# Optimization experiments

Measured on AMD Instinct MI355X. Metric: run time of the kernel, lower is better.

Reference implementation:

```python
import jax, jax.numpy as jnp
import numpy as np

H = 2048       # hidden_size
I = 5504       # intermediate_size
E = 8          # num_experts
TOPK = 2       # num_experts_per_tok


def setup_inputs() -> dict:
    key = jax.random.key(0)
    ks = jax.random.split(key, 5)
    s = 0.02
    x = jax.random.normal(ks[0], (2, 2048, H), dtype=jnp.float32)
    router_w = jax.random.normal(ks[1], (E, H), dtype=jnp.float32) * s   # Linear weight [out,in]
    Wg = jax.random.normal(ks[2], (E, I, H), dtype=jnp.float32) * s      # gate_proj per expert
    Wu = jax.random.normal(ks[3], (E, I, H), dtype=jnp.float32) * s      # up_proj per expert
    Wd = jax.random.normal(ks[4], (E, H, I), dtype=jnp.float32) * s      # down_proj per expert
    return {"x": x, "router_w": router_w, "Wg": Wg, "Wu": Wu, "Wd": Wd}


def reference(x, router_w, Wg, Wu, Wd):
    B, S, Hh = x.shape
    xf = x.reshape(-1, Hh)                                  # [T, H]
    logits = xf @ router_w.T                                # [T, E]
    top_vals, top_idx = jax.lax.top_k(logits, TOPK)         # [T, K]
    top_w = jax.nn.softmax(top_vals, axis=-1)               # softmax over selected logits only
    # combine weight per (token, expert): zero if expert not selected
    combine = jnp.sum(jax.nn.one_hot(top_idx, E, dtype=xf.dtype) * top_w[..., None], axis=1)  # [T, E]

    out = jnp.zeros_like(xf)
    for e in range(E):  # fixed small expert loop (unrolled under jit)
        h = jax.nn.silu(xf @ Wg[e].T) * (xf @ Wu[e].T)      # [T, I]
        y = h @ Wd[e].T                                     # [T, H]
        out = out + combine[:, e:e + 1] * y
    return out.reshape(B, S, Hh)
```

## Files before the change

### kernel.cpp

```cpp
#include <hip/hip_runtime.h>
#include <cstdint>
#include <cstddef>

#define HDIM 2048
#define IDIM 5504
#define NEXP 8
#define NTOK 4096
#define NROWS (2 * NTOK)

#define NCT1 86
#define NRT1 10
#define NWG1 (NCT1 * NRT1 * NEXP)
#define NK1  (HDIM / 32)
#define NCT2 16
#define NRT2 10
#define NWG2 (NCT2 * NRT2 * NEXP)
#define NK2  (IDIM / 32)

typedef _Float16 half8 __attribute__((ext_vector_type(8)));
typedef _Float16 half4v __attribute__((ext_vector_type(4)));
typedef float floatx4 __attribute__((ext_vector_type(4)));

#define GLOAD16(g, l)                                                         \
  __builtin_amdgcn_global_load_lds(                                           \
      (const __attribute__((address_space(1))) void*)(g),                     \
      (__attribute__((address_space(3))) void*)(l), 16, 0, 0)

#define XH_OFF   0
#define HB_OFF   (XH_OFF + (size_t)NTOK * HDIM * 2)
#define BTOK_OFF (HB_OFF + (size_t)NROWS * IDIM * 2)
#define BW_OFF   (BTOK_OFF + 32768)
#define TOKP_OFF (BW_OFF + 32768)
#define TOKW_OFF (TOKP_OFF + 16384)
#define T2R_OFF  (TOKW_OFF + 32768)
#define META_OFF (T2R_OFF + 32768)
#define Y2_OFF   (META_OFF + 128)
#define WD16_OFF (Y2_OFF + (size_t)NROWS * HDIM * 2)


__global__ void cvt_w_kernel(const float4* __restrict__ w, half8* __restrict__ o, int n8) {
  int i = blockIdx.x * blockDim.x + threadIdx.x;
  int st = gridDim.x * blockDim.x;
  for (; i < n8; i += st) {
    float4 a = w[2 * i], b = w[2 * i + 1];
    o[i] = half8{ (_Float16)a.x, (_Float16)a.y, (_Float16)a.z, (_Float16)a.w,
                  (_Float16)b.x, (_Float16)b.y, (_Float16)b.z, (_Float16)b.w };
  }
}

__global__ void router_kernel(const float* __restrict__ x, const float* __restrict__ rw,
                              _Float16* __restrict__ xh,
                              int* __restrict__ tokp, float2* __restrict__ tokw,
                              int* __restrict__ cnt) {
  int t = blockIdx.x * 4 + (threadIdx.x >> 6);
  int lane = threadIdx.x & 63;
  const float4* xr = (const float4*)(x + (size_t)t * HDIM);
  _Float16* xhr = xh + (size_t)t * HDIM;
  float acc[NEXP];
#pragma unroll
  for (int e = 0; e < NEXP; ++e) acc[e] = 0.f;
#pragma unroll
  for (int it = 0; it < HDIM / 256; ++it) {
    float4 xv = xr[lane + 64 * it];
    half4v hv = { (_Float16)xv.x, (_Float16)xv.y, (_Float16)xv.z, (_Float16)xv.w };
    *(half4v*)(xhr + (lane + 64 * it) * 4) = hv;
#pragma unroll
    for (int e = 0; e < NEXP; ++e) {
      float4 wv = ((const float4*)(rw + (size_t)e * HDIM))[lane + 64 * it];
      acc[e] += xv.x * wv.x + xv.y * wv.y + xv.z * wv.z + xv.w * wv.w;
    }
  }
#pragma unroll
  for (int off = 32; off > 0; off >>= 1) {
#pragma unroll
    for (int e = 0; e < NEXP; ++e) acc[e] += __shfl_xor(acc[e], off);
  }
  if (lane == 0) {
    int e0 = 0; float v0 = acc[0];
#pragma unroll
    for (int e = 1; e < NEXP; ++e) {
      if (acc[e] > v0) { v0 = acc[e]; e0 = e; }
    }
    int e1 = -1; float v1 = -3.0e38f;
#pragma unroll
    for (int e = 0; e < NEXP; ++e) {
      if (e == e0) continue;
      if (acc[e] > v1) { v1 = acc[e]; e1 = e; }
    }
    float w0 = 1.f / (1.f + __expf(v1 - v0));
    tokp[t] = e0 | (e1 << 8);
    tokw[t] = make_float2(w0, 1.f - w0);
    atomicAdd(&cnt[e0], 1);
    atomicAdd(&cnt[e1], 1);
  }
}

__global__ void scan_kernel(const int* __restrict__ cnt, int* __restrict__ offp) {
  if (threadIdx.x == 0) {
    int s = 0;
    for (int e = 0; e < NEXP; ++e) { offp[e] = s; s += cnt[e]; }
    offp[NEXP] = s;
  }
}

__global__ void scatter_kernel(const int* __restrict__ tokp, const float2* __restrict__ tokw,
                               const int* __restrict__ offp, int* __restrict__ cursor,
                               int* __restrict__ btok, float* __restrict__ bw,
                               int* __restrict__ t2r) {
  int t = blockIdx.x * blockDim.x + threadIdx.x;
  if (t >= NTOK) return;
  int p = tokp[t];
  float2 w = tokw[t];
  int e0 = p & 0xff, e1 = (p >> 8) & 0xff;
  int r0 = offp[e0] + atomicAdd(&cursor[e0], 1);
  btok[r0] = t; bw[r0] = w.x; t2r[2 * t] = r0;
  int r1 = offp[e1] + atomicAdd(&cursor[e1], 1);
  btok[r1] = t; bw[r1] = w.y; t2r[2 * t + 1] = r1;
}

__global__ void combine_kernel(const _Float16* __restrict__ y2, const int* __restrict__ t2r,
                               const float2* __restrict__ tokw, float* __restrict__ out) {
  int idx = blockIdx.x * 256 + threadIdx.x;
  int t = idx >> 9, c = (idx & 511) * 4;
  int r0 = t2r[2 * t], r1 = t2r[2 * t + 1];
  float2 w = tokw[t];
  half4v v0 = *(const half4v*)(y2 + (size_t)r0 * HDIM + c);
  half4v v1 = *(const half4v*)(y2 + (size_t)r1 * HDIM + c);
  float4 o;
  o.x = w.x * (float)v0[0] + w.y * (float)v1[0];
  o.y = w.x * (float)v0[1] + w.y * (float)v1[1];
  o.z = w.x * (float)v0[2] + w.y * (float)v1[2];
  o.w = w.x * (float)v0[3] + w.y * (float)v1[3];
  *(float4*)(out + (size_t)t * HDIM + c) = o;
}

__global__ __launch_bounds__(256, 3) void stage1_kernel(
    const _Float16* __restrict__ xh, const float* __restrict__ Wg, const float* __restrict__ Wu,
    const int* __restrict__ offp, const int* __restrict__ btok, _Float16* __restrict__ hb) {
  int bid = blockIdx.x;
  int wg = (bid & 7) * (NWG1 / 8) + (bid >> 3);
  int rt = wg % NRT1;
  int ct = (wg / NRT1) % NCT1;
  int e  = wg / (NRT1 * NCT1);
  int base = offp[e];
  int ne = offp[e + 1] - base;
  if (rt * 128 >= ne) return;
  int valid = ne - rt * 128; if (valid > 128) valid = 128;
  int tid = threadIdx.x, lane = tid & 63, wave = tid >> 6;

  __shared__ __attribute__((aligned(16))) _Float16 As[2][128 * 32];
  __shared__ __attribute__((aligned(16))) _Float16 Bs[2][128 * 32];

  const char* abase = (const char*)xh;
  uint32_t aoffB[2];
  const float* bsrc[2];
  int bdstB[2];
  size_t eoff = (size_t)e * IDIM * HDIM;
#pragma unroll
  for (int i = 0; i < 2; ++i) {
    int L = wave * 128 + i * 64 + lane;
    int u = L >> 3, sc = (L & 7) ^ (u & 7);
    int r = 2 * u + (sc >> 2), q = sc & 3;
    int rr = (r < valid) ? r : (valid - 1);
    aoffB[i] = (uint32_t)(((uint32_t)btok[base + rt * 128 + rr] * HDIM + q * 8) * 2);
    const float* rp = (r < 64) ? (Wg + eoff + (size_t)(ct * 64 + r) * HDIM)
                               : (Wu + eoff + (size_t)(ct * 64 + (r - 64)) * HDIM);
    bsrc[i] = rp + q * 8;
    bdstB[i] = L * 16;
  }
  int adst0 = __builtin_amdgcn_readfirstlane(wave * 2048);

  int wm = wave >> 1, wn = wave & 1;
  int lrow = lane & 15, kg = lane >> 4;

  int aoff[4], boff[4];
#pragma unroll
  for (int mi = 0; mi < 4; ++mi) {
    int r = wm * 64 + mi * 16 + lrow;
    int u = r >> 1, cc = (r & 1) * 4 + kg;
    aoff[mi] = u * 64 + ((cc ^ (u & 7)) * 8);
  }
#pragma unroll
  for (int f = 0; f < 4; ++f) {
    int rb = (f < 2) ? (wn * 32 + f * 16 + lrow) : (64 + wn * 32 + (f - 2) * 16 + lrow);
    int u = rb >> 1, cc = (rb & 1) * 4 + kg;
    boff[f] = u * 64 + ((cc ^ (u & 7)) * 8);
  }

  floatx4 acc[4][4] = {};
  floatx4 bp[2][2];

  auto bload = [&](int t) {
#pragma unroll
    for (int i = 0; i < 2; ++i) {
      bp[i][0] = *(const floatx4*)(bsrc[i] + t * 32);
      bp[i][1] = *(const floatx4*)(bsrc[i] + t * 32 + 4);
    }
  };
  auto astage = [&](int t, int buf) {
    uint32_t kb = (uint32_t)t * 64u;
#pragma unroll
    for (int i = 0; i < 2; ++i)
      GLOAD16(abase + (aoffB[i] + kb), (char*)As[buf] + adst0 + i * 1024);
  };
  auto bwrite = [&](int buf) {
#pragma unroll
    for (int i = 0; i < 2; ++i) {
      half8 h = { (_Float16)bp[i][0].x, (_Float16)bp[i][0].y, (_Float16)bp[i][0].z, (_Float16)bp[i][0].w,
                  (_Float16)bp[i][1].x, (_Float16)bp[i][1].y, (_Float16)bp[i][1].z, (_Float16)bp[i][1].w };
      *(half8*)((char*)Bs[buf] + bdstB[i]) = h;
    }
  };
  auto compute = [&](int buf) {
    half8 af[4], bf[4];
#pragma unroll
    for (int mi = 0; mi < 4; ++mi) af[mi] = *(const half8*)&As[buf][aoff[mi]];
#pragma unroll
    for (int f = 0; f < 4; ++f) bf[f] = *(const half8*)&Bs[buf][boff[f]];
#pragma unroll
    for (int mi = 0; mi < 4; ++mi)
#pragma unroll
      for (int f = 0; f < 4; ++f)
        acc[mi][f] = __builtin_amdgcn_mfma_f32_16x16x32_f16(af[mi], bf[f], acc[mi][f], 0, 0, 0);
  };

  int cur = 0;
  bload(0);
  astage(0, 0);
  bwrite(0);
  __syncthreads();
#pragma unroll 2
  for (int t = 0; t < NK1 - 1; ++t) {
    bload(t + 1);
    astage(t + 1, cur ^ 1);
    compute(cur);
    bwrite(cur ^ 1);
    __syncthreads();
    cur ^= 1;
  }
  compute(cur);

  size_t hrow_base = (size_t)(base + rt * 128);
#pragma unroll
  for (int mi = 0; mi < 4; ++mi) {
#pragma unroll
    for (int j = 0; j < 4; ++j) {
      int r = wm * 64 + mi * 16 + kg * 4 + j;
      if (r < valid) {
#pragma unroll
        for (int f = 0; f < 2; ++f) {
          float g = acc[mi][f][j], u = acc[mi][f + 2][j];
          float hv = g / (1.f + __expf(-g)) * u;
          int c = ct * 64 + wn * 32 + f * 16 + lrow;
          hb[(hrow_base + r) * IDIM + c] = (_Float16)hv;
        }
      }
    }
  }
}

__global__ __launch_bounds__(256, 3) void stage2_kernel(
    const _Float16* __restrict__ hb, const _Float16* __restrict__ Wd16,
    const int* __restrict__ offp, _Float16* __restrict__ y2) {
  int bid = blockIdx.x;
  int wg = (bid & 7) * (NWG2 / 8) + (bid >> 3);
  int rt = wg % NRT2;
  int ct = (wg / NRT2) % NCT2;
  int e  = wg / (NRT2 * NCT2);
  int base = offp[e];
  int ne = offp[e + 1] - base;
  if (rt * 128 >= ne) return;
  int valid = ne - rt * 128; if (valid > 128) valid = 128;
  int tid = threadIdx.x, lane = tid & 63, wave = tid >> 6;

  __shared__ __attribute__((aligned(16))) _Float16 As[2][128 * 32];
  __shared__ __attribute__((aligned(16))) _Float16 Bs[2][128 * 32];

  const char* abase = (const char*)hb;
  const char* bbase = (const char*)(Wd16 + (size_t)e * HDIM * IDIM);

  uint32_t aoffB[2], boffB[2];
#pragma unroll
  for (int i = 0; i < 2; ++i) {
    int L = wave * 128 + i * 64 + lane;
    int u = L >> 3, sc = (L & 7) ^ (u & 7);
    int r = 2 * u + (sc >> 2), q = sc & 3;
    int rr = (r < valid) ? r : (valid - 1);
    aoffB[i] = (uint32_t)(((size_t)(base + rt * 128 + rr) * IDIM + (size_t)q * 8) * 2);
    boffB[i] = (uint32_t)(((size_t)(ct * 128 + r) * IDIM + (size_t)q * 8) * 2);
  }
  int adst0 = __builtin_amdgcn_readfirstlane(wave * 2048);

  int wm = wave >> 1, wn = wave & 1;
  int lrow = lane & 15, kg = lane >> 4;

  int aoff[4], boff[4];
#pragma unroll
  for (int mi = 0; mi < 4; ++mi) {
    int r = wm * 64 + mi * 16 + lrow;
    int u = r >> 1, cc = (r & 1) * 4 + kg;
    aoff[mi] = u * 64 + ((cc ^ (u & 7)) * 8);
  }
#pragma unroll
  for (int f = 0; f < 4; ++f) {
    int rb = wn * 64 + f * 16 + lrow;
    int u = rb >> 1, cc = (rb & 1) * 4 + kg;
    boff[f] = u * 64 + ((cc ^ (u & 7)) * 8);
  }

  floatx4 acc[4][4] = {};

  auto stage = [&](int t, int buf) {
    uint32_t kb = (uint32_t)t * 64u;
#pragma unroll
    for (int i = 0; i < 2; ++i) {
      GLOAD16(abase + (aoffB[i] + kb), (char*)As[buf] + adst0 + i * 1024);
      GLOAD16(bbase + (boffB[i] + kb), (char*)Bs[buf] + adst0 + i * 1024);
    }
  };
  auto compute = [&](int buf) {
    half8 af[4], bf[4];
#pragma unroll
    for (int mi = 0; mi < 4; ++mi) af[mi] = *(const half8*)&As[buf][aoff[mi]];
#pragma unroll
    for (int f = 0; f < 4; ++f) bf[f] = *(const half8*)&Bs[buf][boff[f]];
#pragma unroll
    for (int mi = 0; mi < 4; ++mi)
#pragma unroll
      for (int f = 0; f < 4; ++f)
        acc[mi][f] = __builtin_amdgcn_mfma_f32_16x16x32_f16(af[mi], bf[f], acc[mi][f], 0, 0, 0);
  };

  int cur = 0;
  stage(0, 0);
  __syncthreads();
#pragma unroll 2
  for (int t = 0; t < NK2 - 1; ++t) {
    stage(t + 1, cur ^ 1);
    compute(cur);
    __syncthreads();
    cur ^= 1;
  }
  compute(cur);

#pragma unroll
  for (int mi = 0; mi < 4; ++mi) {
#pragma unroll
    for (int j = 0; j < 4; ++j) {
      int r = wm * 64 + mi * 16 + kg * 4 + j;
      if (r < valid) {
        int grow = base + rt * 128 + r;
#pragma unroll
        for (int f = 0; f < 4; ++f) {
          int c = ct * 128 + wn * 64 + f * 16 + lrow;
          y2[(size_t)grow * HDIM + c] = (_Float16)acc[mi][f][j];
        }
      }
    }
  }
}

extern "C" void kernel_launch(void* const* d_in, const int* in_sizes, int n_in,
                              void* d_out, int out_size, void* d_ws, size_t ws_size,
                              hipStream_t stream) {
  const float* x  = (const float*)d_in[0];
  const float* rw = (const float*)d_in[1];
  const float* Wg = (const float*)d_in[2];
  const float* Wu = (const float*)d_in[3];
  const float* Wd = (const float*)d_in[4];
  float* out = (float*)d_out;

  char* ws = (char*)d_ws;
  _Float16* xh  = (_Float16*)(ws + XH_OFF);
  _Float16* hb  = (_Float16*)(ws + HB_OFF);
  int*      btok = (int*)(ws + BTOK_OFF);
  float*    bwv  = (float*)(ws + BW_OFF);
  int*      tokp = (int*)(ws + TOKP_OFF);
  float2*   tokw = (float2*)(ws + TOKW_OFF);
  int*      t2r  = (int*)(ws + T2R_OFF);
  int*      meta = (int*)(ws + META_OFF);
  _Float16* y2   = (_Float16*)(ws + Y2_OFF);
  _Float16* wd16 = (_Float16*)(ws + WD16_OFF);
  int* cnt = meta;
  int* offp = meta + 8;
  int* cursor = meta + 20;

  hipMemsetAsync(meta, 0, 128, stream);

  router_kernel<<<NTOK / 4, 256, 0, stream>>>(x, rw, xh, tokp, tokw, cnt);
  scan_kernel<<<1, 64, 0, stream>>>(cnt, offp);
  scatter_kernel<<<NTOK / 256, 256, 0, stream>>>(tokp, tokw, offp, cursor, btok, bwv, t2r);
  cvt_w_kernel<<<2048, 256, 0, stream>>>((const float4*)Wd, (half8*)wd16,
                                         NEXP * HDIM * IDIM / 8);

  stage1_kernel<<<NWG1, 256, 0, stream>>>(xh, Wg, Wu, offp, btok, hb);
  stage2_kernel<<<NWG2, 256, 0, stream>>>(hb, wd16, offp, y2);
  combine_kernel<<<NTOK * HDIM / 4 / 256, 256, 0, stream>>>(y2, t2r, tokw, out);
}
```

Measured before the change: 1.156 ms.

## Fuse Wd fp16 conversion into stage1 and widen stage2 tiles to 256 columns

Removes the separate Wd conversion kernel. Its grid-stride fp32-to-fp16 conversion now runs at the tail of every stage1 workgroup, including workgroups with no rows, so it overlaps with the GEMM work of other blocks. Stage2 moves to 512-thread blocks with 128x256 tiles, halving the column tiles, so each hidden-activation tile is reused across more output columns. The costs are more LDS per stage2 block, an aggressive launch bound of 6 blocks per CU, and extra memory traffic in stage1 competing with its GEMM loads.

```diff
diff --git a/kernel.cpp b/kernel.cpp
--- a/kernel.cpp
+++ b/kernel.cpp
@@ -12,10 +12,11 @@
 #define NRT1 10
 #define NWG1 (NCT1 * NRT1 * NEXP)
 #define NK1  (HDIM / 32)
-#define NCT2 16
+#define NCT2 8
 #define NRT2 10
 #define NWG2 (NCT2 * NRT2 * NEXP)
 #define NK2  (IDIM / 32)
+#define WDCH (NEXP * HDIM * IDIM / 8)
 
 typedef _Float16 half8 __attribute__((ext_vector_type(8)));
 typedef _Float16 half4v __attribute__((ext_vector_type(4)));
@@ -37,16 +38,6 @@
 #define Y2_OFF   (META_OFF + 128)
 #define WD16_OFF (Y2_OFF + (size_t)NROWS * HDIM * 2)
 
-
-__global__ void cvt_w_kernel(const float4* __restrict__ w, half8* __restrict__ o, int n8) {
-  int i = blockIdx.x * blockDim.x + threadIdx.x;
-  int st = gridDim.x * blockDim.x;
-  for (; i < n8; i += st) {
-    float4 a = w[2 * i], b = w[2 * i + 1];
-    o[i] = half8{ (_Float16)a.x, (_Float16)a.y, (_Float16)a.z, (_Float16)a.w,
-                  (_Float16)b.x, (_Float16)b.y, (_Float16)b.z, (_Float16)b.w };
-  }
-}
 
 __global__ void router_kernel(const float* __restrict__ x, const float* __restrict__ rw,
                               _Float16* __restrict__ xh,
@@ -136,7 +127,8 @@
 
 __global__ __launch_bounds__(256, 3) void stage1_kernel(
     const _Float16* __restrict__ xh, const float* __restrict__ Wg, const float* __restrict__ Wu,
-    const int* __restrict__ offp, const int* __restrict__ btok, _Float16* __restrict__ hb) {
+    const int* __restrict__ offp, const int* __restrict__ btok, _Float16* __restrict__ hb,
+    const float* __restrict__ Wd, _Float16* __restrict__ wd16) {
   int bid = blockIdx.x;
   int wg = (bid & 7) * (NWG1 / 8) + (bid >> 3);
   int rt = wg % NRT1;
@@ -144,122 +136,132 @@
   int e  = wg / (NRT1 * NCT1);
   int base = offp[e];
   int ne = offp[e + 1] - base;
-  if (rt * 128 >= ne) return;
-  int valid = ne - rt * 128; if (valid > 128) valid = 128;
   int tid = threadIdx.x, lane = tid & 63, wave = tid >> 6;
 
-  __shared__ __attribute__((aligned(16))) _Float16 As[2][128 * 32];
-  __shared__ __attribute__((aligned(16))) _Float16 Bs[2][128 * 32];
-
-  const char* abase = (const char*)xh;
-  uint32_t aoffB[2];
-  const float* bsrc[2];
-  int bdstB[2];
-  size_t eoff = (size_t)e * IDIM * HDIM;
-#pragma unroll
-  for (int i = 0; i < 2; ++i) {
-    int L = wave * 128 + i * 64 + lane;
-    int u = L >> 3, sc = (L & 7) ^ (u & 7);
-    int r = 2 * u + (sc >> 2), q = sc & 3;
-    int rr = (r < valid) ? r : (valid - 1);
-    aoffB[i] = (uint32_t)(((uint32_t)btok[base + rt * 128 + rr] * HDIM + q * 8) * 2);
-    const float* rp = (r < 64) ? (Wg + eoff + (size_t)(ct * 64 + r) * HDIM)
-                               : (Wu + eoff + (size_t)(ct * 64 + (r - 64)) * HDIM);
-    bsrc[i] = rp + q * 8;
-    bdstB[i] = L * 16;
-  }
-  int adst0 = __builtin_amdgcn_readfirstlane(wave * 2048);
-
-  int wm = wave >> 1, wn = wave & 1;
-  int lrow = lane & 15, kg = lane >> 4;
-
-  int aoff[4], boff[4];
-#pragma unroll
-  for (int mi = 0; mi < 4; ++mi) {
-    int r = wm * 64 + mi * 16 + lrow;
-    int u = r >> 1, cc = (r & 1) * 4 + kg;
-    aoff[mi] = u * 64 + ((cc ^ (u & 7)) * 8);
-  }
-#pragma unroll
-  for (int f = 0; f < 4; ++f) {
-    int rb = (f < 2) ? (wn * 32 + f * 16 + lrow) : (64 + wn * 32 + (f - 2) * 16 + lrow);
-    int u = rb >> 1, cc = (rb & 1) * 4 + kg;
-    boff[f] = u * 64 + ((cc ^ (u & 7)) * 8);
-  }
-
-  floatx4 acc[4][4] = {};
-  floatx4 bp[2][2];
-
-  auto bload = [&](int t) {
+  if (rt * 128 < ne) {
+    int valid = ne - rt * 128; if (valid > 128) valid = 128;
+
+    __shared__ __attribute__((aligned(16))) _Float16 As[2][128 * 32];
+    __shared__ __attribute__((aligned(16))) _Float16 Bs[2][128 * 32];
+
+    const char* abase = (const char*)xh;
+    uint32_t aoffB[2];
+    const float* bsrc[2];
+    int bdstB[2];
+    size_t eoff = (size_t)e * IDIM * HDIM;
 #pragma unroll
     for (int i = 0; i < 2; ++i) {
-      bp[i][0] = *(const floatx4*)(bsrc[i] + t * 32);
-      bp[i][1] = *(const floatx4*)(bsrc[i] + t * 32 + 4);
-    }
-  };
-  auto astage = [&](int t, int buf) {
-    uint32_t kb = (uint32_t)t * 64u;
-#pragma unroll
-    for (int i = 0; i < 2; ++i)
-      GLOAD16(abase + (aoffB[i] + kb), (char*)As[buf] + adst0 + i * 1024);
-  };
-  auto bwrite = [&](int buf) {
-#pragma unroll
-    for (int i = 0; i < 2; ++i) {
-      half8 h = { (_Float16)bp[i][0].x, (_Float16)bp[i][0].y, (_Float16)bp[i][0].z, (_Float16)bp[i][0].w,
-                  (_Float16)bp[i][1].x, (_Float16)bp[i][1].y, (_Float16)bp[i][1].z, (_Float16)bp[i][1].w };
-      *(half8*)((char*)Bs[buf] + bdstB[i]) = h;
-    }
-  };
-  auto compute = [&](int buf) {
-    half8 af[4], bf[4];
-#pragma unroll
-    for (int mi = 0; mi < 4; ++mi) af[mi] = *(const half8*)&As[buf][aoff[mi]];
-#pragma unroll
-    for (int f = 0; f < 4; ++f) bf[f] = *(const half8*)&Bs[buf][boff[f]];
-#pragma unroll
-    for (int mi = 0; mi < 4; ++mi)
-#pragma unroll
-      for (int f = 0; f < 4; ++f)
-        acc[mi][f] = __builtin_amdgcn_mfma_f32_16x16x32_f16(af[mi], bf[f], acc[mi][f], 0, 0, 0);
-  };
-
-  int cur = 0;
-  bload(0);
-  astage(0, 0);
-  bwrite(0);
-  __syncthreads();
+      int L = wave * 128 + i * 64 + lane;
+      int u = L >> 3, sc = (L & 7) ^ (u & 7);
+      int r = 2 * u + (sc >> 2), q = sc & 3;
+      int rr = (r < valid) ? r : (valid - 1);
+      aoffB[i] = (uint32_t)(((uint32_t)btok[base + rt * 128 + rr] * HDIM + q * 8) * 2);
+      const float* rp = (r < 64) ? (Wg + eoff + (size_t)(ct * 64 + r) * HDIM)
+                                 : (Wu + eoff + (size_t)(ct * 64 + (r - 64)) * HDIM);
+      bsrc[i] = rp + q * 8;
+      bdstB[i] = L * 16;
+    }
+    int adst0 = __builtin_amdgcn_readfirstlane(wave * 2048);
+
+    int wm = wave >> 1, wn = wave & 1;
+    int lrow = lane & 15, kg = lane >> 4;
+
+    int aoff[4], boff[4];
+#pragma unroll
+    for (int mi = 0; mi < 4; ++mi) {
+      int r = wm * 64 + mi * 16 + lrow;
+      int u = r >> 1, cc = (r & 1) * 4 + kg;
+      aoff[mi] = u * 64 + ((cc ^ (u & 7)) * 8);
+    }
+#pragma unroll
+    for (int f = 0; f < 4; ++f) {
+      int rb = (f < 2) ? (wn * 32 + f * 16 + lrow) : (64 + wn * 32 + (f - 2) * 16 + lrow);
+      int u = rb >> 1, cc = (rb & 1) * 4 + kg;
+      boff[f] = u * 64 + ((cc ^ (u & 7)) * 8);
+    }
+
+    floatx4 acc[4][4] = {};
+    floatx4 bp[2][2];
+
+    auto bload = [&](int t) {
+#pragma unroll
+      for (int i = 0; i < 2; ++i) {
+        bp[i][0] = *(const floatx4*)(bsrc[i] + t * 32);
+        bp[i][1] = *(const floatx4*)(bsrc[i] + t * 32 + 4);
+      }
+    };
+    auto astage = [&](int t, int buf) {
+      uint32_t kb = (uint32_t)t * 64u;
+#pragma unroll
+      for (int i = 0; i < 2; ++i)
+        GLOAD16(abase + (aoffB[i] + kb), (char*)As[buf] + adst0 + i * 1024);
+    };
+    auto bwrite = [&](int buf) {
+#pragma unroll
+      for (int i = 0; i < 2; ++i) {
+        half8 h = { (_Float16)bp[i][0].x, (_Float16)bp[i][0].y, (_Float16)bp[i][0].z, (_Float16)bp[i][0].w,
+                    (_Float16)bp[i][1].x, (_Float16)bp[i][1].y, (_Float16)bp[i][1].z, (_Float16)bp[i][1].w };
+        *(half8*)((char*)Bs[buf] + bdstB[i]) = h;
+      }
+    };
+    auto compute = [&](int buf) {
+      half8 af[4], bf[4];
+#pragma unroll
+      for (int mi = 0; mi < 4; ++mi) af[mi] = *(const half8*)&As[buf][aoff[mi]];
+#pragma unroll
+      for (int f = 0; f < 4; ++f) bf[f] = *(const half8*)&Bs[buf][boff[f]];
+#pragma unroll
+      for (int mi = 0; mi < 4; ++mi)
+#pragma unroll
+        for (int f = 0; f < 4; ++f)
+          acc[mi][f] = __builtin_amdgcn_mfma_f32_16x16x32_f16(af[mi], bf[f], acc[mi][f], 0, 0, 0);
+    };
+
+    int cur = 0;
+    bload(0);
+    astage(0, 0);
+    bwrite(0);
+    __syncthreads();
 #pragma unroll 2
-  for (int t = 0; t < NK1 - 1; ++t) {
-    bload(t + 1);
-    astage(t + 1, cur ^ 1);
+    for (int t = 0; t < NK1 - 1; ++t) {
+      bload(t + 1);
+      astage(t + 1, cur ^ 1);
+      compute(cur);
+      bwrite(cur ^ 1);
+      __syncthreads();
+      cur ^= 1;
+    }
     compute(cur);
-    bwrite(cur ^ 1);
-    __syncthreads();
-    cur ^= 1;
-  }
-  compute(cur);
-
-  size_t hrow_base = (size_t)(base + rt * 128);
-#pragma unroll
-  for (int mi = 0; mi < 4; ++mi) {
-#pragma unroll
-    for (int j = 0; j < 4; ++j) {
-      int r = wm * 64 + mi * 16 + kg * 4 + j;
-      if (r < valid) {
-#pragma unroll
-        for (int f = 0; f < 2; ++f) {
-          float g = acc[mi][f][j], u = acc[mi][f + 2][j];
-          float hv = g / (1.f + __expf(-g)) * u;
-          int c = ct * 64 + wn * 32 + f * 16 + lrow;
-          hb[(hrow_base + r) * IDIM + c] = (_Float16)hv;
+
+    size_t hrow_base = (size_t)(base + rt * 128);
+#pragma unroll
+    for (int mi = 0; mi < 4; ++mi) {
+#pragma unroll
+      for (int j = 0; j < 4; ++j) {
+        int r = wm * 64 + mi * 16 + kg * 4 + j;
+        if (r < valid) {
+#pragma unroll
+          for (int f = 0; f < 2; ++f) {
+            float g = acc[mi][f][j], u = acc[mi][f + 2][j];
+            float hv = g / (1.f + __expf(-g)) * u;
+            int c = ct * 64 + wn * 32 + f * 16 + lrow;
+            hb[(hrow_base + r) * IDIM + c] = (_Float16)hv;
+          }
         }
       }
     }
   }
-}
-
-__global__ __launch_bounds__(256, 3) void stage2_kernel(
+
+  const float4* wsrc = (const float4*)Wd;
+  half8* wdst = (half8*)wd16;
+  for (int i = bid * 256 + tid; i < WDCH; i += NWG1 * 256) {
+    float4 a = wsrc[2 * i], b = wsrc[2 * i + 1];
+    wdst[i] = half8{ (_Float16)a.x, (_Float16)a.y, (_Float16)a.z, (_Float16)a.w,
+                     (_Float16)b.x, (_Float16)b.y, (_Float16)b.z, (_Float16)b.w };
+  }
+}
+
+__global__ __launch_bounds__(512, 6) void stage2_kernel(
     const _Float16* __restrict__ hb, const _Float16* __restrict__ Wd16,
     const int* __restrict__ offp, _Float16* __restrict__ y2) {
   int bid = blockIdx.x;
@@ -274,24 +276,29 @@
   int tid = threadIdx.x, lane = tid & 63, wave = tid >> 6;
 
   __shared__ __attribute__((aligned(16))) _Float16 As[2][128 * 32];
-  __shared__ __attribute__((aligned(16))) _Float16 Bs[2][128 * 32];
+  __shared__ __attribute__((aligned(16))) _Float16 Bs[2][256 * 32];
 
   const char* abase = (const char*)hb;
   const char* bbase = (const char*)(Wd16 + (size_t)e * HDIM * IDIM);
 
-  uint32_t aoffB[2], boffB[2];
-#pragma unroll
-  for (int i = 0; i < 2; ++i) {
-    int L = wave * 128 + i * 64 + lane;
+  uint32_t aoffB, boffB[2];
+  {
+    int L = tid;
     int u = L >> 3, sc = (L & 7) ^ (u & 7);
     int r = 2 * u + (sc >> 2), q = sc & 3;
     int rr = (r < valid) ? r : (valid - 1);
-    aoffB[i] = (uint32_t)(((size_t)(base + rt * 128 + rr) * IDIM + (size_t)q * 8) * 2);
-    boffB[i] = (uint32_t)(((size_t)(ct * 128 + r) * IDIM + (size_t)q * 8) * 2);
-  }
-  int adst0 = __builtin_amdgcn_readfirstlane(wave * 2048);
-
-  int wm = wave >> 1, wn = wave & 1;
+    aoffB = (uint32_t)(((size_t)(base + rt * 128 + rr) * IDIM + (size_t)q * 8) * 2);
+  }
+#pragma unroll
+  for (int i = 0; i < 2; ++i) {
+    int L = i * 512 + tid;
+    int u = L >> 3, sc = (L & 7) ^ (u & 7);
+    int r = 2 * u + (sc >> 2), q = sc & 3;
+    boffB[i] = (uint32_t)(((size_t)(ct * 256 + r) * IDIM + (size_t)q * 8) * 2);
+  }
+  int adst0 = __builtin_amdgcn_readfirstlane(wave * 1024);
+
+  int wm = wave >> 2, wn = wave & 3;
   int lrow = lane & 15, kg = lane >> 4;
 
   int aoff[4], boff[4];
@@ -312,11 +319,10 @@
 
   auto stage = [&](int t, int buf) {
     uint32_t kb = (uint32_t)t * 64u;
-#pragma unroll
-    for (int i = 0; i < 2; ++i) {
-      GLOAD16(abase + (aoffB[i] + kb), (char*)As[buf] + adst0 + i * 1024);
-      GLOAD16(bbase + (boffB[i] + kb), (char*)Bs[buf] + adst0 + i * 1024);
-    }
+    GLOAD16(abase + (aoffB + kb), (char*)As[buf] + adst0);
+#pragma unroll
+    for (int i = 0; i < 2; ++i)
+      GLOAD16(bbase + (boffB[i] + kb), (char*)Bs[buf] + i * 8192 + adst0);
   };
   auto compute = [&](int buf) {
     half8 af[4], bf[4];
@@ -352,7 +358,7 @@
         int grow = base + rt * 128 + r;
 #pragma unroll
         for (int f = 0; f < 4; ++f) {
-          int c = ct * 128 + wn * 64 + f * 16 + lrow;
+          int c = ct * 256 + wn * 64 + f * 16 + lrow;
           y2[(size_t)grow * HDIM + c] = (_Float16)acc[mi][f][j];
         }
       }
@@ -390,10 +396,8 @@
   router_kernel<<<NTOK / 4, 256, 0, stream>>>(x, rw, xh, tokp, tokw, cnt);
   scan_kernel<<<1, 64, 0, stream>>>(cnt, offp);
   scatter_kernel<<<NTOK / 256, 256, 0, stream>>>(tokp, tokw, offp, cursor, btok, bwv, t2r);
-  cvt_w_kernel<<<2048, 256, 0, stream>>>((const float4*)Wd, (half8*)wd16,
-                                         NEXP * HDIM * IDIM / 8);
-
-  stage1_kernel<<<NWG1, 256, 0, stream>>>(xh, Wg, Wu, offp, btok, hb);
-  stage2_kernel<<<NWG2, 256, 0, stream>>>(hb, wd16, offp, y2);
+
+  stage1_kernel<<<NWG1, 256, 0, stream>>>(xh, Wg, Wu, offp, btok, hb, Wd, wd16);
+  stage2_kernel<<<NWG2, 512, 0, stream>>>(hb, wd16, offp, y2);
   combine_kernel<<<NTOK * HDIM / 4 / 256, 256, 0, stream>>>(y2, t2r, tokw, out);
 }
```

New measurement: 2.066 ms. +78.7%, slower.
